# Performance work log

Hardware: AMD Instinct MI355X
Metric: run time of the kernel (lower is better)

The kernel has to match this reference:

```python
import jax, jax.numpy as jnp
import numpy as np
from jax import lax

WIN = 7          # win_size
K1 = 0.01
K2 = 0.03
NP_W = WIN * WIN
COV_NORM = NP_W / (NP_W - 1)


def _box_filter(x):
    w = jnp.ones((1, 1, WIN, WIN), x.dtype) / NP_W
    return lax.conv_general_dilated(
        x, w, window_strides=(1, 1), padding='VALID',
        dimension_numbers=('NCHW', 'OIHW', 'NCHW'))


def setup_inputs() -> dict:
    key = jax.random.key(0)
    k1, k2 = jax.random.split(key)
    B, C, T, H, W = 16, 1, 20, 256, 256
    Xt = jax.random.uniform(k1, (B, C, T, H, W), dtype=jnp.float32)
    Yt = jax.random.uniform(k2, (B, C, T, H, W), dtype=jnp.float32)
    data_range = jnp.ones((1,), dtype=jnp.float32)  # unused: overwritten per frame
    return {"Xt": Xt, "Yt": Yt, "data_range": data_range}


def reference(Xt, Yt, data_range):
    B, C, T, H, W = Xt.shape
    # Fold time into batch: frame index = b*T + t
    X = Xt.transpose(0, 2, 1, 3, 4).reshape(B * T, C, H, W)
    Y = Yt.transpose(0, 2, 1, 3, 4).reshape(B * T, C, H, W)

    # Per-frame data_range = max over the whole batch slice Yt[:,:,t]
    # (torch.Tensor([Y.max()]) detaches it from autograd in the original)
    dr = lax.stop_gradient(jnp.max(Yt, axis=(0, 1, 3, 4)))      # [T]
    dr = jnp.tile(dr, B)[:, None, None, None]                   # [B*T,1,1,1]
    C1 = (K1 * dr) ** 2
    C2 = (K2 * dr) ** 2

    # One conv call over 5 stacked moment maps
    stacked = jnp.concatenate([X, Y, X * X, Y * Y, X * Y], axis=0)
    filt = _box_filter(stacked)
    ux, uy, uxx, uyy, uxy = jnp.split(filt, 5, axis=0)

    vx = COV_NORM * (uxx - ux * ux)
    vy = COV_NORM * (uyy - uy * uy)
    vxy = COV_NORM * (uxy - ux * uy)

    A1 = 2 * ux * uy + C1
    A2 = 2 * vxy + C2
    B1 = ux * ux + uy * uy + C1
    B2 = vx + vy + C2
    S = (A1 * A2) / (B1 * B2)

    # sum_t (1 - mean(S_t)) / T == 1 - mean(S) since every frame has equal count
    return 1.0 - jnp.mean(S)
```

## Files before the change

kernel.cpp:

```cpp
#include <hip/hip_runtime.h>


#define HH 256
#define WW 256
#define OUTW 250
#define NT 20
#define NB 16
#define NFRAMES (NT * NB)
#define STRIPS 25
#define RPS 10
#define NWAVES (NFRAMES * STRIPS)
#define WPB 4
#define NBLK2 (NWAVES / WPB)

__device__ __forceinline__ float wave_sum(float v) {
#pragma unroll
    for (int off = 32; off > 0; off >>= 1) v += __shfl_down(v, off, 64);
    return v;
}
__device__ __forceinline__ float wave_max(float v) {
#pragma unroll
    for (int off = 32; off > 0; off >>= 1) v = fmaxf(v, __shfl_down(v, off, 64));
    return v;
}

__global__ __launch_bounds__(256) void dr_max_kernel(const float* __restrict__ Y,
                                                     unsigned* __restrict__ dr_bits) {
    int t = blockIdx.x;
    int bq = blockIdx.y;
    const float4* p = (const float4*)(Y + (size_t)((bq >> 2) * NT + t) * (HH * WW))
                      + (bq & 3) * 4096;
    float m = 0.f;
#pragma unroll 4
    for (int k = 0; k < 16; ++k) {
        float4 v = p[k * 256 + threadIdx.x];
        m = fmaxf(m, fmaxf(fmaxf(v.x, v.y), fmaxf(v.z, v.w)));
    }
    m = wave_max(m);
    __shared__ float smax[4];
    int lane = threadIdx.x & 63, w = threadIdx.x >> 6;
    if (lane == 0) smax[w] = m;
    __syncthreads();
    if (threadIdx.x == 0) {
        float mm = fmaxf(fmaxf(smax[0], smax[1]), fmaxf(smax[2], smax[3]));
        atomicMax(dr_bits + t, __float_as_uint(mm));
    }
}


__device__ __forceinline__ float ssim_px(float hx, float hy, float hxx, float hyy,
                                         float hxy, float c1, float c2) {
    const float cov = 49.0f / 48.0f;
    float hx2 = hx * hx, hy2 = hy * hy, hxy1 = hx * hy;
    float A1 = __builtin_fmaf(2.f, hxy1, c1);
    float B1 = hx2 + hy2 + c1;
    float t1 = __builtin_fmaf(49.f, hxx, -hx2);
    float t2 = __builtin_fmaf(49.f, hyy, -hy2);
    float t3 = __builtin_fmaf(49.f, hxy, -hxy1);
    float A2 = __builtin_fmaf(2.f * cov, t3, c2);
    float B2 = __builtin_fmaf(cov, t1 + t2, c2);
    return (A1 * A2) * __builtin_amdgcn_rcpf(B1 * B2);
}

__device__ __forceinline__ float4 taps7_shfl(float4 s) {
    float P  = (s.x + s.y) + (s.z + s.w);
    float P1 = __shfl_down(P,   1, 64);
    float w1 = __shfl_down(s.w, 1, 64);
    float x2 = __shfl_down(s.x, 2, 64);
    float y2 = __shfl_down(s.y, 2, 64);
    float base = P + P1;
    float o0 = base - w1;
    float o1 = base - s.x;
    float o2 = s.z + s.w + P1 + x2;
    float o3 = o2 - s.z + y2;
    return make_float4(o0, o1, o2, o3);
}

__device__ __forceinline__ void slide5(float4& sx, float4& sy, float4& sxx,
                                       float4& syy, float4& sxy,
                                       float4 xo, float4 yo, float4 xn, float4 yn) {
    sx.x += xn.x - xo.x; sx.y += xn.y - xo.y; sx.z += xn.z - xo.z; sx.w += xn.w - xo.w;
    sy.x += yn.x - yo.x; sy.y += yn.y - yo.y; sy.z += yn.z - yo.z; sy.w += yn.w - yo.w;
    sxx.x += xn.x * xn.x - xo.x * xo.x; sxx.y += xn.y * xn.y - xo.y * xo.y;
    sxx.z += xn.z * xn.z - xo.z * xo.z; sxx.w += xn.w * xn.w - xo.w * xo.w;
    syy.x += yn.x * yn.x - yo.x * yo.x; syy.y += yn.y * yn.y - yo.y * yo.y;
    syy.z += yn.z * yn.z - yo.z * yo.z; syy.w += yn.w * yn.w - yo.w * yo.w;
    sxy.x += xn.x * yn.x - xo.x * yo.x; sxy.y += xn.y * yn.y - xo.y * yo.y;
    sxy.z += xn.z * yn.z - xo.z * yo.z; sxy.w += xn.w * yn.w - xo.w * yo.w;
}

__global__ __launch_bounds__(256, 4) void ssim_kernel(const float* __restrict__ X,
                                                      const float* __restrict__ Y,
                                                      const float* __restrict__ dr_arr,
                                                      float* __restrict__ partials) {
    int w = threadIdx.x >> 6;
    int l = threadIdx.x & 63;
    int wid = blockIdx.x * WPB + w;
    int frame = wid / STRIPS;
    int strip = wid % STRIPS;
    int t = frame % NT;
    const float4* x4 = (const float4*)(X + (size_t)frame * (HH * WW));
    const float4* y4 = (const float4*)(Y + (size_t)frame * (HH * WW));
    int c0 = 4 * l;

    float dr = dr_arr[t];
    float c1 = 2401.f * (0.01f * dr) * (0.01f * dr);
    float c2 = 2401.f * (0.03f * dr) * (0.03f * dr);

    int r0 = strip * RPS;

    float4 sx = make_float4(0, 0, 0, 0), sy = sx, sxx = sx, syy = sx, sxy = sx;
#pragma unroll
    for (int dy = 0; dy < 7; ++dy) {
        float4 xv = x4[(r0 + dy) * 64 + l];
        float4 yv = y4[(r0 + dy) * 64 + l];
        sx.x += xv.x; sx.y += xv.y; sx.z += xv.z; sx.w += xv.w;
        sy.x += yv.x; sy.y += yv.y; sy.z += yv.z; sy.w += yv.w;
        sxx.x += xv.x * xv.x; sxx.y += xv.y * xv.y; sxx.z += xv.z * xv.z; sxx.w += xv.w * xv.w;
        syy.x += yv.x * yv.x; syy.y += yv.y * yv.y; syy.z += yv.z * yv.z; syy.w += yv.w * yv.w;
        sxy.x += xv.x * yv.x; sxy.y += xv.y * yv.y; sxy.z += xv.z * yv.z; sxy.w += xv.w * yv.w;
    }

    float acc = 0.f;
    for (int it = 0; it < RPS; ++it) {
        int r = r0 + it;
        bool last = (it == RPS - 1);

        float4 xo, yo, xn, yn;
        if (!last) {
            xo = x4[r * 64 + l];       yo = y4[r * 64 + l];
            xn = x4[(r + 7) * 64 + l]; yn = y4[(r + 7) * 64 + l];
        }

        float4 hx  = taps7_shfl(sx);
        float4 hy  = taps7_shfl(sy);
        float4 hxx = taps7_shfl(sxx);
        float4 hyy = taps7_shfl(syy);
        float4 hxy = taps7_shfl(sxy);

        if (c0 + 0 < OUTW) acc += ssim_px(hx.x, hy.x, hxx.x, hyy.x, hxy.x, c1, c2);
        if (c0 + 1 < OUTW) acc += ssim_px(hx.y, hy.y, hxx.y, hyy.y, hxy.y, c1, c2);
        if (c0 + 2 < OUTW) acc += ssim_px(hx.z, hy.z, hxx.z, hyy.z, hxy.z, c1, c2);
        if (c0 + 3 < OUTW) acc += ssim_px(hx.w, hy.w, hxx.w, hyy.w, hxy.w, c1, c2);

        if (!last)
            slide5(sx, sy, sxx, syy, sxy, xo, yo, xn, yn);
    }

    acc = wave_sum(acc);
    if (l == 0) partials[wid] = acc;
}

__global__ __launch_bounds__(256) void final_kernel(const float* __restrict__ partials,
                                                    float* __restrict__ out) {
    float s = 0.f;
    for (int i = threadIdx.x; i < NWAVES; i += 256) s += partials[i];
    s = wave_sum(s);
    __shared__ float ssum[4];
    int lane = threadIdx.x & 63, w = threadIdx.x >> 6;
    if (lane == 0) ssum[w] = s;
    __syncthreads();
    if (threadIdx.x == 0) {
        float total = ssum[0] + ssum[1] + ssum[2] + ssum[3];
        const double denom = (double)NFRAMES * OUTW * OUTW;
        out[0] = (float)(1.0 - (double)total / denom);
    }
}

extern "C" void kernel_launch(void* const* d_in, const int* in_sizes, int n_in,
                              void* d_out, int out_size, void* d_ws, size_t ws_size,
                              hipStream_t stream) {
    const float* X = (const float*)d_in[0];
    const float* Y = (const float*)d_in[1];

    float* ws = (float*)d_ws;
    unsigned* dr_bits = (unsigned*)ws;
    float* partials   = ws + 32;

    hipMemsetAsync(d_ws, 0, NT * sizeof(float), stream);

    dim3 g1(NT, NB * 4);
    hipLaunchKernelGGL(dr_max_kernel, g1, dim3(256), 0, stream, Y, dr_bits);
    hipLaunchKernelGGL(ssim_kernel, dim3(NBLK2), dim3(256), 0, stream,
                       X, Y, (const float*)ws, partials);
    hipLaunchKernelGGL(final_kernel, dim3(1), dim3(256), 0, stream,
                       partials, (float*)d_out);
}
```

Measured before the change: 217.7 us.

## Drop memset and atomics, halve strip height, swizzle blocks across XCDs

The data-range max now writes per-block partial maxima to a 64-slot array per frame time, and each SSIM wave reduces them itself with a shuffle. This removes the memset launch and the atomicMax. Strips shrink from 10 to 5 output rows, doubling the number of waves. That gives more parallelism but makes the 6-row vertical halo a larger share of each strip's reads. Block IDs are swizzled so that consecutive strips of a frame land on the same XCD, which is meant to improve L2 reuse of the overlapping rows.

```diff
diff --git a/kernel.cpp b/kernel.cpp
--- a/kernel.cpp
+++ b/kernel.cpp
@@ -7,25 +7,21 @@
 #define NT 20
 #define NB 16
 #define NFRAMES (NT * NB)
-#define STRIPS 25
-#define RPS 10
+#define STRIPS 50
+#define RPS 5
 #define NWAVES (NFRAMES * STRIPS)
 #define WPB 4
 #define NBLK2 (NWAVES / WPB)
+#define NXCD 8
 
 __device__ __forceinline__ float wave_sum(float v) {
 #pragma unroll
     for (int off = 32; off > 0; off >>= 1) v += __shfl_down(v, off, 64);
     return v;
 }
-__device__ __forceinline__ float wave_max(float v) {
-#pragma unroll
-    for (int off = 32; off > 0; off >>= 1) v = fmaxf(v, __shfl_down(v, off, 64));
-    return v;
-}
 
 __global__ __launch_bounds__(256) void dr_max_kernel(const float* __restrict__ Y,
-                                                     unsigned* __restrict__ dr_bits) {
+                                                     float* __restrict__ dr_part) {
     int t = blockIdx.x;
     int bq = blockIdx.y;
     const float4* p = (const float4*)(Y + (size_t)((bq >> 2) * NT + t) * (HH * WW))
@@ -36,15 +32,14 @@
         float4 v = p[k * 256 + threadIdx.x];
         m = fmaxf(m, fmaxf(fmaxf(v.x, v.y), fmaxf(v.z, v.w)));
     }
-    m = wave_max(m);
+#pragma unroll
+    for (int off = 32; off > 0; off >>= 1) m = fmaxf(m, __shfl_down(m, off, 64));
     __shared__ float smax[4];
     int lane = threadIdx.x & 63, w = threadIdx.x >> 6;
     if (lane == 0) smax[w] = m;
     __syncthreads();
-    if (threadIdx.x == 0) {
-        float mm = fmaxf(fmaxf(smax[0], smax[1]), fmaxf(smax[2], smax[3]));
-        atomicMax(dr_bits + t, __float_as_uint(mm));
-    }
+    if (threadIdx.x == 0)
+        dr_part[t * 64 + bq] = fmaxf(fmaxf(smax[0], smax[1]), fmaxf(smax[2], smax[3]));
 }
 
 
@@ -91,11 +86,13 @@
 
 __global__ __launch_bounds__(256, 4) void ssim_kernel(const float* __restrict__ X,
                                                       const float* __restrict__ Y,
-                                                      const float* __restrict__ dr_arr,
+                                                      const float* __restrict__ dr_part,
                                                       float* __restrict__ partials) {
     int w = threadIdx.x >> 6;
     int l = threadIdx.x & 63;
-    int wid = blockIdx.x * WPB + w;
+    int bid = blockIdx.x;
+    int swz = (bid % NXCD) * (NBLK2 / NXCD) + bid / NXCD;
+    int wid = swz * WPB + w;
     int frame = wid / STRIPS;
     int strip = wid % STRIPS;
     int t = frame % NT;
@@ -103,7 +100,9 @@
     const float4* y4 = (const float4*)(Y + (size_t)frame * (HH * WW));
     int c0 = 4 * l;
 
-    float dr = dr_arr[t];
+    float dr = dr_part[t * 64 + l];
+#pragma unroll
+    for (int off = 32; off > 0; off >>= 1) dr = fmaxf(dr, __shfl_xor(dr, off, 64));
     float c1 = 2401.f * (0.01f * dr) * (0.01f * dr);
     float c2 = 2401.f * (0.03f * dr) * (0.03f * dr);
 
@@ -174,15 +173,13 @@
     const float* Y = (const float*)d_in[1];
 
     float* ws = (float*)d_ws;
-    unsigned* dr_bits = (unsigned*)ws;
-    float* partials   = ws + 32;
-
-    hipMemsetAsync(d_ws, 0, NT * sizeof(float), stream);
+    float* dr_part  = ws;
+    float* partials = ws + 2048;
 
     dim3 g1(NT, NB * 4);
-    hipLaunchKernelGGL(dr_max_kernel, g1, dim3(256), 0, stream, Y, dr_bits);
+    hipLaunchKernelGGL(dr_max_kernel, g1, dim3(256), 0, stream, Y, dr_part);
     hipLaunchKernelGGL(ssim_kernel, dim3(NBLK2), dim3(256), 0, stream,
-                       X, Y, (const float*)ws, partials);
+                       X, Y, (const float*)dr_part, partials);
     hipLaunchKernelGGL(final_kernel, dim3(1), dim3(256), 0, stream,
                        partials, (float*)d_out);
 }
```

New measurement: 210.5 us. 3.3% less time.
